# Kernel optimization log

Measured on AMD Instinct MI355X. Metric: run time of the kernel, lower is better.

## Reference

```python
import jax, jax.numpy as jnp
import numpy as np

BETA = 25.0  # torch nn.Softplus(beta=25.0)

def softplus_b(z):
    return jax.nn.softplus(BETA * z) / BETA

def setup_inputs() -> dict:
    key = jax.random.key(0)
    ks = jax.random.split(key, 9)
    B, H = 16384, 512
    def lin_init(kw, kb, out_f, in_f):
        bound = 1.0 / np.sqrt(in_f)
        W = jax.random.uniform(kw, (out_f, in_f), jnp.float32, -bound, bound)
        b = jax.random.uniform(kb, (out_f,), jnp.float32, -bound, bound)
        return W, b
    W0, b0 = lin_init(ks[1], ks[2], H, 4)
    W1, b1 = lin_init(ks[3], ks[4], H, H)
    W2, b2 = lin_init(ks[5], ks[6], H, H)
    W3, b3 = lin_init(ks[7], ks[8], 5, H)
    x = jax.random.normal(ks[0], (B, 4), jnp.float32)
    return {"x": x, "W0": W0, "b0": b0, "W1": W1, "b1": b1,
            "W2": W2, "b2": b2, "W3": W3, "b3": b3}

def reference(x, W0, b0, W1, b1, W2, b2, W3, b3):
    def net(z):  # (4,) -> (5,)
        h = softplus_b(W0 @ z + b0)
        h = softplus_b(W1 @ h + b1)
        h = softplus_b(W2 @ h + b2)
        return W3 @ h + b3

    def A_matrix(z):  # antisymmetrized Jacobian of first 4 outputs, (4,4)
        J = jax.jacrev(lambda p: net(p)[:4])(z)
        return J - J.T

    def point_trace(z):
        # T[i,j,k] = d A[i,j] / d z[k]; torch einsum('...ii') -> sum_j T[i,j,j]
        T = jax.jacfwd(A_matrix)(z)  # (4,4,4)
        return jnp.einsum('ijj->i', T)  # (4,)

    trace = jax.vmap(point_trace)(x)          # (B,4)
    u = jax.vmap(net)(x)                      # (B,5)
    return jnp.concatenate([trace, u[:, 4:5]], axis=1)  # (B,5)
```

## Files before the change

kernel.cpp:

```cpp
#include <hip/hip_runtime.h>
#include <math.h>

#define HDIM 512
#define NCH 16
#define BETA 25.0f
#define NKH 48

typedef unsigned short ushort_t;
typedef __attribute__((ext_vector_type(8))) short short8;
typedef __attribute__((ext_vector_type(4))) float f32x4;

__device__ __forceinline__ ushort_t f2bf(float f) {
    unsigned u = __float_as_uint(f);
    unsigned r = (u + 0x7fff + ((u >> 16) & 1)) >> 16;
    return (ushort_t)r;
}
__device__ __forceinline__ float bf2f(ushort_t b) {
    return __uint_as_float(((unsigned)b) << 16);
}
__device__ __forceinline__ void split_bf(float v, ushort_t& hi, ushort_t& lo) {
    hi = f2bf(v);
    lo = f2bf(v - bf2f(hi));
}

__device__ __forceinline__ void softplus_jet(float v, float& phi, float& s, float& pp) {
    float y = BETA * v;
    float e = expf(-fabsf(y));
    float inv = 1.0f / (1.0f + e);
    s = (y >= 0.0f) ? inv : e * inv;
    phi = (fmaxf(y, 0.0f) + log1pf(e)) * (1.0f / BETA);
    pp = BETA * s * (1.0f - s);
}

__device__ __forceinline__ void gl_lds16(const void* g, void* l) {
    __builtin_amdgcn_global_load_lds(
        (const __attribute__((address_space(1))) unsigned int*)g,
        (__attribute__((address_space(3))) unsigned int*)l, 16, 0, 0);
}

__global__ __launch_bounds__(256) void layer0_jet(
    const float* __restrict__ x, const float* __restrict__ W0,
    const float* __restrict__ b0, ushort_t* __restrict__ A0)
{
    __shared__ ushort_t sm[16 * 1024];
    int p = blockIdx.x, tid = threadIdx.x;
    float4 z = *reinterpret_cast<const float4*>(&x[p * 4]);
#pragma unroll
    for (int half = 0; half < 2; ++half) {
        int n = half * 256 + tid;
        float4 w = *reinterpret_cast<const float4*>(&W0[n * 4]);
        float v = fmaf(w.x, z.x, fmaf(w.y, z.y, fmaf(w.z, z.z, fmaf(w.w, z.w, b0[n]))));
        float phi, s, pp;
        softplus_jet(v, phi, s, pp);
        float wa[4] = {w.x, w.y, w.z, w.w};
        float o[16];
        o[0] = phi;
#pragma unroll
        for (int a = 0; a < 4; ++a) o[1 + a] = s * wa[a];
        int idx = 5;
#pragma unroll
        for (int a = 0; a < 4; ++a)
#pragma unroll
            for (int b = a; b < 4; ++b) { o[idx] = pp * wa[a] * wa[b]; ++idx; }
        o[15] = 0.0f;
#pragma unroll
        for (int c = 0; c < 16; ++c) {
            ushort_t hb, lb;
            split_bf(o[c], hb, lb);
            sm[c * 1024 + n] = hb;
            sm[c * 1024 + 512 + n] = lb;
        }
    }
    __syncthreads();
    uint4* d4 = reinterpret_cast<uint4*>(A0 + (size_t)p * 16 * 1024);
    const uint4* s4 = reinterpret_cast<const uint4*>(sm);
#pragma unroll
    for (int i = 0; i < 8; ++i) d4[tid + 256 * i] = s4[tid + 256 * i];
}

template<int EPI>
__global__ __launch_bounds__(512, 2) void gemm_jet9(
    const ushort_t* __restrict__ Ag, const ushort_t* __restrict__ BT,
    const float* __restrict__ bias, ushort_t* __restrict__ Anext,
    float* __restrict__ Sout)
{
    __shared__ char smem[98304];
    ushort_t* Asl = (ushort_t*)smem;
    ushort_t* Bsl = (ushort_t*)(smem + 49152);
    float*    epi = (float*)smem;

    const int tid = threadIdx.x;
    const int wave = tid >> 6, lane = tid & 63;
    const int wr = wave >> 2, wc = wave & 3;

    int nwg = gridDim.x, bid = blockIdx.x;
    int q = nwg >> 3, r = nwg & 7;
    int xcd = bid & 7, i8 = bid >> 3;
    int logical = (xcd < r ? xcd * (q + 1) : r * (q + 1) + (xcd - r) * q) + i8;
    const int mt = logical >> 1;
    const int m0 = mt * 256;
    const int n0 = (logical & 1) * 256;

    const int s_c = (((lane & 3) - ((lane >> 3) & 3)) & 3) * 8;

    f32x4 acc[8][4] = {};

    auto kaof = [](int g) { return (g < 32) ? (g >> 1) * 32 : 512 + (g - 32) * 32; };
    auto kbof = [](int g) { return (g < 32) ? ((g & 1) << 9) + (g >> 1) * 32 : (g - 32) * 32; };

    auto stageA = [&](int g, int slot) {
        if (g >= NKH) g = 0;
        int ka = kaof(g);
#pragma unroll
        for (int rr = 0; rr < 2; ++rr) {
            int row = rr * 128 + wave * 16 + (lane >> 2);
            gl_lds16(Ag + (size_t)(m0 + row) * 1024 + ka + s_c,
                     Asl + slot * 8192 + rr * 4096 + wave * 512);
        }
    };
    auto stageB = [&](int g, int slot) {
        if (g >= NKH) g = 0;
        int kb = kbof(g);
#pragma unroll
        for (int rr = 0; rr < 2; ++rr) {
            int row = rr * 128 + wave * 16 + (lane >> 2);
            gl_lds16(BT + (size_t)(n0 + row) * 1024 + kb + s_c,
                     Bsl + slot * 8192 + rr * 4096 + wave * 512);
        }
    };

    const int rA = lane & 15;
    const int rd = rA * 32 + ((((lane >> 4) + (rA >> 1)) & 3) * 8);

    stageA(0, 0); stageB(0, 0); stageA(1, 1); stageB(1, 1);
    asm volatile("s_waitcnt vmcnt(4)" ::: "memory");
    __builtin_amdgcn_s_barrier();
    asm volatile("" ::: "memory");

    short8 afA[4], afB[4], bfr[4];
#pragma unroll
    for (int mi = 0; mi < 4; ++mi)
        afA[mi] = *(const short8*)&Asl[(wr * 128 + mi * 16) * 32 + rd];
#pragma unroll
    for (int ni = 0; ni < 4; ++ni)
        bfr[ni] = *(const short8*)&Bsl[(wc * 64 + ni * 16) * 32 + rd];

    for (int gj = 0; gj < 16; ++gj) {
#pragma unroll
        for (int u = 0; u < 3; ++u) {
            const int g = gj * 3 + u;
            const int s  = u;
            const int s1 = (u + 1) % 3;
            const int s2 = (u + 2) % 3;
#pragma unroll
            for (int mi = 0; mi < 4; ++mi)
                afB[mi] = *(const short8*)&Asl[s * 8192 + (wr * 128 + 64 + mi * 16) * 32 + rd];
            stageA(g + 2, s2);
            asm volatile("s_waitcnt vmcnt(4)" ::: "memory");
            __builtin_amdgcn_s_barrier();
            __builtin_amdgcn_s_setprio(1);
#pragma unroll
            for (int mi = 0; mi < 4; ++mi)
#pragma unroll
                for (int ni = 0; ni < 4; ++ni)
                    acc[mi][ni] = __builtin_amdgcn_mfma_f32_16x16x32_bf16(
                        afA[mi], bfr[ni], acc[mi][ni], 0, 0, 0);
            __builtin_amdgcn_s_setprio(0);
            asm volatile("" ::: "memory");
            __builtin_amdgcn_s_barrier();
            asm volatile("" ::: "memory");
#pragma unroll
            for (int mi = 0; mi < 4; ++mi)
                afA[mi] = *(const short8*)&Asl[s1 * 8192 + (wr * 128 + mi * 16) * 32 + rd];
            stageB(g + 2, s2);
            asm volatile("s_waitcnt vmcnt(4)" ::: "memory");
            __builtin_amdgcn_s_barrier();
            __builtin_amdgcn_s_setprio(1);
#pragma unroll
            for (int mi = 0; mi < 4; ++mi)
#pragma unroll
                for (int ni = 0; ni < 4; ++ni)
                    acc[4 + mi][ni] = __builtin_amdgcn_mfma_f32_16x16x32_bf16(
                        afB[mi], bfr[ni], acc[4 + mi][ni], 0, 0, 0);
            __builtin_amdgcn_s_setprio(0);
#pragma unroll
            for (int ni = 0; ni < 4; ++ni)
                bfr[ni] = *(const short8*)&Bsl[s1 * 8192 + (wc * 64 + ni * 16) * 32 + rd];
            asm volatile("" ::: "memory");
            __builtin_amdgcn_s_barrier();
            asm volatile("" ::: "memory");
        }
    }

    asm volatile("s_waitcnt vmcnt(0) lgkmcnt(0)" ::: "memory");
    __builtin_amdgcn_s_barrier();
    asm volatile("" ::: "memory");

    const int pl = lane & 15, ph = lane >> 4;
    const int wxor = (ph & 1) << 4;
#pragma unroll
    for (int h = 0; h < 4; ++h) {
        if (h) { asm volatile("" ::: "memory"); __builtin_amdgcn_s_barrier(); }
        if (wr == (h >> 1)) {
            const int ab = (h & 1) * 4;
#pragma unroll
            for (int lm = 0; lm < 4; ++lm)
#pragma unroll
                for (int ni = 0; ni < 4; ++ni)
#pragma unroll
                    for (int rr = 0; rr < 4; ++rr)
                        epi[(lm * 16 + ph * 4 + rr) * 256 + ((wc * 64 + ni * 16 + pl) ^ wxor)] = acc[ab + lm][ni][rr];
        }
        asm volatile("" ::: "memory");
        __builtin_amdgcn_s_barrier();
        asm volatile("" ::: "memory");
#pragma unroll
        for (int rep = 0; rep < 2; ++rep) {
            int idx = rep * 512 + tid;
            int n = idx & 255, pq = idx >> 8;
            const float* vp = &epi[pq * 16 * 256];
            float v[15];
#pragma unroll
            for (int c = 0; c < 15; ++c) v[c] = vp[c * 256 + (n ^ (((c >> 2) & 1) << 4))];
            float val = v[0] + bias[n0 + n];
            float phi, s, pp;
            softplus_jet(val, phi, s, pp);
            float o[16];
            o[0] = phi;
            float d[4];
#pragma unroll
            for (int a = 0; a < 4; ++a) { d[a] = v[1 + a]; o[1 + a] = s * d[a]; }
            int ix = 5;
#pragma unroll
            for (int a = 0; a < 4; ++a)
#pragma unroll
                for (int b = a; b < 4; ++b) { o[ix] = pp * d[a] * d[b] + s * v[ix]; ++ix; }
            o[15] = 0.0f;
            size_t prow = (size_t)mt * 16 + h * 4 + pq;
            if (EPI == 1) {
                size_t rb = prow * 16 * 1024;
#pragma unroll
                for (int c = 0; c < 16; ++c) {
                    ushort_t hb, lb;
                    split_bf(o[c], hb, lb);
                    Anext[rb + (size_t)c * 1024 + n0 + n] = hb;
                    Anext[rb + (size_t)c * 1024 + 512 + n0 + n] = lb;
                }
            } else {
                float4* op = reinterpret_cast<float4*>(Sout + ((size_t)prow * 512 + n0 + n) * 16);
#pragma unroll
                for (int qq = 0; qq < 4; ++qq)
                    op[qq] = make_float4(o[4*qq], o[4*qq+1], o[4*qq+2], o[4*qq+3]);
            }
        }
    }
}

__global__ __launch_bounds__(256) void trace_kernel(
    const float* __restrict__ Sin, const float* __restrict__ W3,
    const float* __restrict__ b3, float* __restrict__ out, int npts)
{
    int wave = threadIdx.x >> 6;
    int lane = threadIdx.x & 63;
    int p = blockIdx.x * 4 + wave;
    if (p >= npts) return;
    const float* sp = Sin + (size_t)p * (HDIM * NCH);

    float hu[4][10];
#pragma unroll
    for (int m = 0; m < 4; ++m)
#pragma unroll
        for (int qq = 0; qq < 10; ++qq) hu[m][qq] = 0.0f;
    float u4 = 0.0f;

    for (int kk = 0; kk < 8; ++kk) {
        int k = kk * 64 + lane;
        const float* sk = sp + k * NCH;
        float4 s0 = *reinterpret_cast<const float4*>(&sk[0]);
        float4 s1 = *reinterpret_cast<const float4*>(&sk[4]);
        float4 s2 = *reinterpret_cast<const float4*>(&sk[8]);
        float4 s3 = *reinterpret_cast<const float4*>(&sk[12]);
        float hv[10] = {s1.y,s1.z,s1.w, s2.x,s2.y,s2.z,s2.w, s3.x,s3.y,s3.z};
        float w3m[5];
#pragma unroll
        for (int m = 0; m < 5; ++m) w3m[m] = W3[m * HDIM + k];
        u4 = fmaf(w3m[4], s0.x, u4);
#pragma unroll
        for (int m = 0; m < 4; ++m)
#pragma unroll
            for (int qq = 0; qq < 10; ++qq) hu[m][qq] = fmaf(w3m[m], hv[qq], hu[m][qq]);
    }

#pragma unroll
    for (int off = 32; off > 0; off >>= 1) {
#pragma unroll
        for (int m = 0; m < 4; ++m)
#pragma unroll
            for (int qq = 0; qq < 10; ++qq) hu[m][qq] += __shfl_xor(hu[m][qq], off, 64);
        u4 += __shfl_xor(u4, off, 64);
    }

    if (lane == 0) {
        const int Pm[4][4] = {{0,1,2,3},{1,4,5,6},{2,5,7,8},{3,6,8,9}};
        const int Pd[4] = {0, 4, 7, 9};
#pragma unroll
        for (int i = 0; i < 4; ++i) {
            float t1 = hu[i][Pd[0]] + hu[i][Pd[1]] + hu[i][Pd[2]] + hu[i][Pd[3]];
            float t2 = hu[0][Pm[0][i]] + hu[1][Pm[1][i]] + hu[2][Pm[2][i]] + hu[3][Pm[3][i]];
            out[p * 5 + i] = t1 - t2;
        }
        out[p * 5 + 4] = u4 + b3[4];
    }
}

__global__ void prep_B(const float* __restrict__ W1, const float* __restrict__ W2,
                       ushort_t* __restrict__ BT1, ushort_t* __restrict__ BT2)
{
    int tid = blockIdx.x * 256 + threadIdx.x;
    int l = tid >> 18;
    int i = tid & 262143;
    int n = i >> 9, k = i & 511;
    const float* W = l ? W2 : W1;
    ushort_t* BT = l ? BT2 : BT1;
    float v = W[i];
    ushort_t hb, lb;
    split_bf(v, hb, lb);
    size_t rr = (size_t)n * 1024;
    BT[rr + k] = hb;
    BT[rr + 512 + k] = lb;
}

extern "C" void kernel_launch(void* const* d_in, const int* in_sizes, int n_in,
                              void* d_out, int out_size, void* d_ws, size_t ws_size,
                              hipStream_t stream)
{
    const float* x  = (const float*)d_in[0];
    const float* W0 = (const float*)d_in[1];
    const float* b0 = (const float*)d_in[2];
    const float* W1 = (const float*)d_in[3];
    const float* b1 = (const float*)d_in[4];
    const float* W2 = (const float*)d_in[5];
    const float* b2 = (const float*)d_in[6];
    const float* W3 = (const float*)d_in[7];
    const float* b3 = (const float*)d_in[8];
    float* out = (float*)d_out;

    int B = in_sizes[0] / 4;

    ushort_t* BT1 = (ushort_t*)d_ws;
    ushort_t* BT2 = BT1 + 512 * 1024;
    char* bufbase = (char*)(BT2 + 512 * 1024);

    size_t avail = ws_size - 2ull * 512 * 1024 * sizeof(ushort_t);
    size_t per_pt = 2ull * 32768;
    int Pc = (int)(avail / per_pt) & ~15;
    if (Pc > 16384) Pc = 16384;
    if (Pc < 16) Pc = 16;

    ushort_t* A0 = (ushort_t*)bufbase;
    ushort_t* A1 = (ushort_t*)(bufbase + (size_t)Pc * 32768);
    float* S2 = (float*)A0;

    prep_B<<<2048, 256, 0, stream>>>(W1, W2, BT1, BT2);

    for (int base = 0; base < B; base += Pc) {
        int np = (B - base < Pc) ? (B - base) : Pc;
        layer0_jet<<<np, 256, 0, stream>>>(x + (size_t)base * 4, W0, b0, A0);
        int nwg = (np / 16) * 2;
        gemm_jet9<1><<<nwg, 512, 0, stream>>>(A0, BT1, b1, A1, nullptr);
        gemm_jet9<2><<<nwg, 512, 0, stream>>>(A1, BT2, b2, nullptr, S2);
        trace_kernel<<<(np + 3) / 4, 256, 0, stream>>>(S2, W3, b3, out + (size_t)base * 5, np);
    }
}
```

Baseline: 1.314 ms.

## Switch GEMM main loop to 4-slot LDS ring with one barrier per k-step

```diff
diff --git a/kernel.cpp b/kernel.cpp
--- a/kernel.cpp
+++ b/kernel.cpp
@@ -79,14 +79,14 @@
 }
 
 template<int EPI>
-__global__ __launch_bounds__(512, 2) void gemm_jet9(
+__global__ __launch_bounds__(512, 2) void gemm_jet10(
     const ushort_t* __restrict__ Ag, const ushort_t* __restrict__ BT,
     const float* __restrict__ bias, ushort_t* __restrict__ Anext,
     float* __restrict__ Sout)
 {
-    __shared__ char smem[98304];
+    __shared__ char smem[131072];
     ushort_t* Asl = (ushort_t*)smem;
-    ushort_t* Bsl = (ushort_t*)(smem + 49152);
+    ushort_t* Bsl = (ushort_t*)(smem + 65536);
     float*    epi = (float*)smem;
 
     const int tid = threadIdx.x;
@@ -133,61 +133,42 @@
     const int rd = rA * 32 + ((((lane >> 4) + (rA >> 1)) & 3) * 8);
 
     stageA(0, 0); stageB(0, 0); stageA(1, 1); stageB(1, 1);
-    asm volatile("s_waitcnt vmcnt(4)" ::: "memory");
-    __builtin_amdgcn_s_barrier();
-    asm volatile("" ::: "memory");
-
-    short8 afA[4], afB[4], bfr[4];
-#pragma unroll
-    for (int mi = 0; mi < 4; ++mi)
-        afA[mi] = *(const short8*)&Asl[(wr * 128 + mi * 16) * 32 + rd];
-#pragma unroll
-    for (int ni = 0; ni < 4; ++ni)
-        bfr[ni] = *(const short8*)&Bsl[(wc * 64 + ni * 16) * 32 + rd];
-
-    for (int gj = 0; gj < 16; ++gj) {
-#pragma unroll
-        for (int u = 0; u < 3; ++u) {
-            const int g = gj * 3 + u;
+
+    for (int gj = 0; gj < 12; ++gj) {
+#pragma unroll
+        for (int u = 0; u < 4; ++u) {
+            const int g = gj * 4 + u;
             const int s  = u;
-            const int s1 = (u + 1) % 3;
-            const int s2 = (u + 2) % 3;
-#pragma unroll
-            for (int mi = 0; mi < 4; ++mi)
-                afB[mi] = *(const short8*)&Asl[s * 8192 + (wr * 128 + 64 + mi * 16) * 32 + rd];
+            const int s2 = (u + 2) & 3;
             stageA(g + 2, s2);
-            asm volatile("s_waitcnt vmcnt(4)" ::: "memory");
-            __builtin_amdgcn_s_barrier();
-            __builtin_amdgcn_s_setprio(1);
-#pragma unroll
-            for (int mi = 0; mi < 4; ++mi)
-#pragma unroll
-                for (int ni = 0; ni < 4; ++ni)
-                    acc[mi][ni] = __builtin_amdgcn_mfma_f32_16x16x32_bf16(
-                        afA[mi], bfr[ni], acc[mi][ni], 0, 0, 0);
-            __builtin_amdgcn_s_setprio(0);
-            asm volatile("" ::: "memory");
-            __builtin_amdgcn_s_barrier();
-            asm volatile("" ::: "memory");
-#pragma unroll
-            for (int mi = 0; mi < 4; ++mi)
-                afA[mi] = *(const short8*)&Asl[s1 * 8192 + (wr * 128 + mi * 16) * 32 + rd];
             stageB(g + 2, s2);
             asm volatile("s_waitcnt vmcnt(4)" ::: "memory");
             __builtin_amdgcn_s_barrier();
+            asm volatile("" ::: "memory");
+            short8 bf[4], a0[4], a1[4];
+#pragma unroll
+            for (int ni = 0; ni < 4; ++ni)
+                bf[ni] = *(const short8*)&Bsl[s * 8192 + (wc * 64 + ni * 16) * 32 + rd];
+#pragma unroll
+            for (int mi = 0; mi < 4; ++mi)
+                a0[mi] = *(const short8*)&Asl[s * 8192 + (wr * 128 + mi * 16) * 32 + rd];
+#pragma unroll
+            for (int mi = 0; mi < 4; ++mi)
+                a1[mi] = *(const short8*)&Asl[s * 8192 + (wr * 128 + 64 + mi * 16) * 32 + rd];
             __builtin_amdgcn_s_setprio(1);
+#pragma unroll
+            for (int mi = 0; mi < 4; ++mi)
+#pragma unroll
+                for (int ni = 0; ni < 4; ++ni)
+                    acc[mi][ni] = __builtin_amdgcn_mfma_f32_16x16x32_bf16(
+                        a0[mi], bf[ni], acc[mi][ni], 0, 0, 0);
 #pragma unroll
             for (int mi = 0; mi < 4; ++mi)
 #pragma unroll
                 for (int ni = 0; ni < 4; ++ni)
                     acc[4 + mi][ni] = __builtin_amdgcn_mfma_f32_16x16x32_bf16(
-                        afB[mi], bfr[ni], acc[4 + mi][ni], 0, 0, 0);
+                        a1[mi], bf[ni], acc[4 + mi][ni], 0, 0, 0);
             __builtin_amdgcn_s_setprio(0);
-#pragma unroll
-            for (int ni = 0; ni < 4; ++ni)
-                bfr[ni] = *(const short8*)&Bsl[s1 * 8192 + (wc * 64 + ni * 16) * 32 + rd];
-            asm volatile("" ::: "memory");
-            __builtin_amdgcn_s_barrier();
             asm volatile("" ::: "memory");
         }
     }
@@ -367,8 +348,8 @@
         int np = (B - base < Pc) ? (B - base) : Pc;
         layer0_jet<<<np, 256, 0, stream>>>(x + (size_t)base * 4, W0, b0, A0);
         int nwg = (np / 16) * 2;
-        gemm_jet9<1><<<nwg, 512, 0, stream>>>(A0, BT1, b1, A1, nullptr);
-        gemm_jet9<2><<<nwg, 512, 0, stream>>>(A1, BT2, b2, nullptr, S2);
+        gemm_jet10<1><<<nwg, 512, 0, stream>>>(A0, BT1, b1, A1, nullptr);
+        gemm_jet10<2><<<nwg, 512, 0, stream>>>(A1, BT2, b2, nullptr, S2);
         trace_kernel<<<(np + 3) / 4, 256, 0, stream>>>(S2, W3, b3, out + (size_t)base * 5, np);
     }
 }
```

Measured after the change: 1.313 ms. About the same (-0.1%).
